# Optimization experiments

Measured on AMD Instinct MI355X. Metric: run time of the kernel, lower is better.

The kernel has to match this reference:

```python
import jax, jax.numpy as jnp
import numpy as np

B, C, H, W = 2, 512, 48, 48
HEADS = 8          # head_dim = C // HEADS = 64
GROUPS = 32        # min(32, ceil(512/4)) = 32
EPS = 1e-5


def setup_inputs() -> dict:
    key = jax.random.key(0)
    ks = jax.random.split(key, 5)
    return {
        "x": jax.random.normal(ks[0], (B, C, H, W), jnp.float32),
        "gn_w": jnp.ones((C,), jnp.float32),
        "gn_b": jnp.zeros((C,), jnp.float32),
        # 1x1 convs stored as [out, in] matrices
        "qkv_w": jax.random.normal(ks[1], (3 * C, C), jnp.float32) / np.float32(np.sqrt(C)),
        "qkv_b": jax.random.normal(ks[2], (3 * C,), jnp.float32) * 0.01,
        "proj_w": jax.random.normal(ks[3], (C, C), jnp.float32) / np.float32(np.sqrt(C)),
        "proj_b": jax.random.normal(ks[4], (C,), jnp.float32) * 0.01,
    }


def _group_norm(x, w, b):
    b_, c_, h_, w_ = x.shape
    xg = x.reshape(b_, GROUPS, c_ // GROUPS, h_, w_)
    mean = xg.mean(axis=(2, 3, 4), keepdims=True)
    var = xg.var(axis=(2, 3, 4), keepdims=True)  # biased, matches F.group_norm
    xn = ((xg - mean) * jax.lax.rsqrt(var + EPS)).reshape(b_, c_, h_, w_)
    return xn * w[None, :, None, None] + b[None, :, None, None]


def reference(x, gn_w, gn_b, qkv_w, qkv_b, proj_w, proj_b):
    bx, cx, hx, wx = x.shape
    d = cx // HEADS
    n = hx * wx
    xn = _group_norm(x, gn_w, gn_b)
    # qkv 1x1 conv -> [B, 3C, H, W]
    y = jnp.einsum('oc,bchw->bohw', qkv_w, xn) + qkv_b[None, :, None, None]
    # torch: y.reshape(B*heads, d, 3, N).unbind(2)  (channel layout: head, chan, qkv)
    qkv = y.reshape(bx * HEADS, d, 3, n)
    q, k, v = qkv[:, :, 0, :], qkv[:, :, 1, :], qkv[:, :, 2, :]
    scale = np.float32(1.0 / np.sqrt(d))
    # AttentionOp: fp32 QK^T + softmax over keys (axis=2)
    w_attn = jax.nn.softmax(jnp.einsum('ncq,nck->nqk', q, k * scale), axis=2)
    a = jnp.einsum('nqk,nck->ncq', w_attn, v).reshape(bx, cx, hx, wx)
    out = jnp.einsum('oc,bchw->bohw', proj_w, a) + proj_b[None, :, None, None]
    return out + x
```

## Files before the change

kernel.cpp:

```cpp
#include <hip/hip_runtime.h>

typedef __bf16 bf16;
typedef __bf16 bf16x8 __attribute__((ext_vector_type(8)));
typedef __bf16 bf16x4 __attribute__((ext_vector_type(4)));
typedef float f32x4 __attribute__((ext_vector_type(4)));

#define B_ 2
#define C_ 512
#define HW_ 2304
#define GROUPS_ 32
#define CPG_ 16
#define EPS_ 1e-5f
#define THR_ 8.0f
#define LOG2E_ 1.44269504f
#define EXP2(x) __builtin_amdgcn_exp2f(x)

__device__ __forceinline__ void gload_lds16(const bf16* g, bf16* l) {
  __builtin_amdgcn_global_load_lds((const __attribute__((address_space(1))) void*)g,
                                   (__attribute__((address_space(3))) void*)l, 16, 0, 0);
}

__global__ __launch_bounds__(256) void gn_stats_part_k(const float* __restrict__ x,
                                                       float* __restrict__ ps,
                                                       float* __restrict__ pss) {
  int blk = blockIdx.x;
  int bg = blk >> 3, seg = blk & 7;
  const int n4 = CPG_ * HW_ / 4 / 8;
  const float4* p = (const float4*)(x + (long)bg * CPG_ * HW_) + (long)seg * n4;
  float s = 0.f, ss = 0.f;
  for (int i = threadIdx.x; i < n4; i += 256) {
    float4 v = p[i];
    s += v.x + v.y + v.z + v.w;
    ss += v.x * v.x + v.y * v.y + v.z * v.z + v.w * v.w;
  }
#pragma unroll
  for (int d = 1; d < 64; d <<= 1) { s += __shfl_xor(s, d); ss += __shfl_xor(ss, d); }
  __shared__ float rs[4], rss[4];
  int wave = threadIdx.x >> 6, lane = threadIdx.x & 63;
  if (lane == 0) { rs[wave] = s; rss[wave] = ss; }
  __syncthreads();
  if (threadIdx.x == 0) {
    ps[blk] = rs[0] + rs[1] + rs[2] + rs[3];
    pss[blk] = rss[0] + rss[1] + rss[2] + rss[3];
  }
}

__global__ __launch_bounds__(256) void gn_apply_k(const float* __restrict__ x,
                                                  const float* __restrict__ gw,
                                                  const float* __restrict__ gb,
                                                  const float* __restrict__ ps,
                                                  const float* __restrict__ pss,
                                                  bf16* __restrict__ xnT) {
  int n0 = blockIdx.x * 64, c0 = blockIdx.y * 32, b = blockIdx.z;
  int nn = n0 + (threadIdx.x & 63);
  int cb = c0 + ((threadIdx.x >> 6) << 3);
  int gi = b * GROUPS_ + (cb >> 4);
  float s = 0.f, ss = 0.f;
#pragma unroll
  for (int k = 0; k < 8; ++k) { s += ps[gi * 8 + k]; ss += pss[gi * 8 + k]; }
  const float invN = 1.0f / (float)(CPG_ * HW_);
  float mu = s * invN;
  float var = ss * invN - mu * mu;
  float rstd = rsqrtf(var + EPS_);
  bf16x8 o;
#pragma unroll
  for (int j = 0; j < 8; ++j) {
    int c = cb + j;
    float sc = rstd * gw[c];
    float sh = gb[c] - mu * sc;
    float v = x[((long)b * C_ + c) * HW_ + nn];
    o[j] = (bf16)(v * sc + sh);
  }
  *(bf16x8*)&xnT[((long)b * HW_ + nn) * C_ + cb] = o;
}

__global__ __launch_bounds__(256) void prep_w_k(const float* __restrict__ qkv_w,
                                                const float* __restrict__ qkv_b,
                                                const float* __restrict__ proj_w,
                                                bf16* __restrict__ wqk,
                                                bf16* __restrict__ wv,
                                                bf16* __restrict__ wp,
                                                float* __restrict__ bqk,
                                                float* __restrict__ bv) {
  int idx = blockIdx.x * 256 + threadIdx.x;
  int r = idx >> 9, c = idx & 511;
  {
    int src = (r < 512) ? 3 * r : 3 * (r - 512) + 1;
    float sc = (r < 512) ? 0.125f * LOG2E_ : 1.0f;
    wqk[idx] = (bf16)(qkv_w[(long)src * 512 + c] * sc);
  }
  if (r < 512) {
    wv[idx] = (bf16)(qkv_w[(long)(3 * r + 2) * 512 + c]);
    wp[idx] = (bf16)(proj_w[idx]);
  }
  if (idx < 1024) {
    int src = (idx < 512) ? 3 * idx : 3 * (idx - 512) + 1;
    float sc = (idx < 512) ? 0.125f * LOG2E_ : 1.0f;
    bqk[idx] = qkv_b[src] * sc;
  }
  if (idx < 512) bv[idx] = qkv_b[3 * idx + 2];
}

template <int BIAS_MODE, bool RESID, typename OUT_T>
__global__ __launch_bounds__(256) void gemm_k(const bf16* __restrict__ A,
                                              const bf16* __restrict__ BT,
                                              const float* __restrict__ bias,
                                              const float* __restrict__ resid,
                                              OUT_T* __restrict__ Cc,
                                              int M, int N,
                                              long sA, long sBT, long sC) {
  constexpr int KK = 512;
  constexpr int NSTEP = KK >> 5;
  int b = blockIdx.z;
  A += sA * b;
  BT += sBT * b;
  Cc += sC * b;
  const float* R = RESID ? (resid + sC * b) : nullptr;
  int m0 = blockIdx.y * 64, n0 = blockIdx.x * 64;
  int tid = threadIdx.x, lane = tid & 63, wave = tid >> 6;
  int wm = (wave >> 1) << 5, wn = (wave & 1) << 5;
  int fr = lane & 15, kg = (lane >> 4) << 3;
  __shared__ __align__(16) bf16 As[3][64 * 32];
  __shared__ __align__(16) bf16 Bs[3][64 * 32];
  int sr = tid >> 2, sc = (tid & 3) << 3;
  const bf16* gA = A + (long)(m0 + sr) * KK + sc;
  const bf16* gB = BT + (long)(n0 + sr) * KK + sc;
  f32x4 acc[2][2] = {};
  gload_lds16(gA, &As[0][tid * 8]);
  gload_lds16(gB, &Bs[0][tid * 8]);
  gload_lds16(gA + 32, &As[1][tid * 8]);
  gload_lds16(gB + 32, &Bs[1][tid * 8]);
  asm volatile("s_waitcnt vmcnt(2)" ::: "memory");
  __builtin_amdgcn_s_barrier();
#pragma unroll
  for (int t = 0; t < NSTEP; ++t) {
    const int cur = t % 3;
    if (t + 2 < NSTEP) {
      const int nb = (t + 2) % 3;
      int k0 = (t + 2) << 5;
      gload_lds16(gA + k0, &As[nb][tid * 8]);
      gload_lds16(gB + k0, &Bs[nb][tid * 8]);
    }
    bf16x8 a0 = *(bf16x8*)&As[cur][(wm + fr) * 32 + kg];
    bf16x8 a1 = *(bf16x8*)&As[cur][(wm + 16 + fr) * 32 + kg];
    bf16x8 b0 = *(bf16x8*)&Bs[cur][(wn + fr) * 32 + kg];
    bf16x8 b1 = *(bf16x8*)&Bs[cur][(wn + 16 + fr) * 32 + kg];
    acc[0][0] = __builtin_amdgcn_mfma_f32_16x16x32_bf16(a0, b0, acc[0][0], 0, 0, 0);
    acc[0][1] = __builtin_amdgcn_mfma_f32_16x16x32_bf16(a0, b1, acc[0][1], 0, 0, 0);
    acc[1][0] = __builtin_amdgcn_mfma_f32_16x16x32_bf16(a1, b0, acc[1][0], 0, 0, 0);
    acc[1][1] = __builtin_amdgcn_mfma_f32_16x16x32_bf16(a1, b1, acc[1][1], 0, 0, 0);
    if (t + 2 < NSTEP) {
      asm volatile("s_waitcnt vmcnt(2) lgkmcnt(0)" ::: "memory");
    } else if (t + 1 < NSTEP) {
      asm volatile("s_waitcnt vmcnt(0) lgkmcnt(0)" ::: "memory");
    }
    if (t + 1 < NSTEP) __builtin_amdgcn_s_barrier();
  }
  int rbase = (lane >> 4) << 2;
#pragma unroll
  for (int mi = 0; mi < 2; ++mi)
#pragma unroll
    for (int nj = 0; nj < 2; ++nj)
#pragma unroll
      for (int reg = 0; reg < 4; ++reg) {
        int row = m0 + wm + (mi << 4) + rbase + reg;
        int col = n0 + wn + (nj << 4) + fr;
        float v = acc[mi][nj][reg];
        if (BIAS_MODE == 1) v += bias[row];
        if (BIAS_MODE == 2) v += bias[col];
        if (RESID) v += R[(long)row * N + col];
        Cc[(long)row * N + col] = (OUT_T)v;
      }
}

template <int NS>
__global__ __launch_bounds__(512) void attn_k(const bf16* __restrict__ yT,
                                              const bf16* __restrict__ V,
                                              bf16* __restrict__ Op,
                                              float* __restrict__ Mp,
                                              float* __restrict__ Lp) {
  const int n = HW_;
  constexpr int NT = (HW_ / NS) / 64;
  int bh = blockIdx.y, b = bh >> 3, h = bh & 7;
  int split = blockIdx.z;
  int q0 = blockIdx.x * 128;
  int kbeg = split * (n / NS);
  int tid = threadIdx.x, lane = tid & 63, wave = tid >> 6;
  int fr = lane & 15, g = lane >> 4, kg = g << 3;
  const bf16* yTb = yT + (long)b * n * 1024;
  const bf16* Vb = V + ((long)b * C_ + h * 64) * n;
  const bf16* Kb = yTb + 512 + h * 64;

  int qrow = q0 + (wave << 4) + fr;
  const bf16* qp = yTb + (long)qrow * 1024 + h * 64;
  bf16x8 qf0 = *(const bf16x8*)(qp + kg);
  bf16x8 qf1 = *(const bf16x8*)(qp + 32 + kg);

  __shared__ __align__(16) bf16 Kt[2][64][64];
  __shared__ __align__(16) bf16 Vt[2][64][64];

  int o0 = ((g + fr) & 7) << 3;
  int o1 = ((4 + g + fr) & 7) << 3;

  float m_run = -1e30f, l_run = 0.f;
  f32x4 oacc[4] = {};

  int r0 = tid >> 3;
  int ck = tid & 7;
  int c0e = ck << 3;
  int pk = ((ck + r0) & 7) << 3;
  int vs = (c0e & 32) | ((c0e & 8) << 1) | ((c0e & 16) >> 2);
  int cv = vs >> 3, sub = vs & 7;
  int pv0 = (((cv + r0) & 7) << 3) + sub;
  int pv1 = (((cv + 1 + r0) & 7) << 3) + sub;

  const bf16* kptr = Kb + (long)(kbeg + r0) * 1024 + c0e;
  const bf16* vptr = Vb + (long)r0 * n + kbeg + c0e;
  uint4 rk = *(const uint4*)kptr;
  uint4 rv = *(const uint4*)vptr;
  *(uint4*)&Kt[0][r0][pk] = rk;
  *(uint2*)&Vt[0][r0][pv0] = make_uint2(rv.x, rv.y);
  *(uint2*)&Vt[0][r0][pv1] = make_uint2(rv.z, rv.w);
  kptr += 64 * 1024;
  vptr += 64;
  rk = *(const uint4*)kptr;
  rv = *(const uint4*)vptr;
  __syncthreads();

  for (int t = 0; t < NT; ++t) {
    int cur = t & 1;
    f32x4 s[4] = {};
    __builtin_amdgcn_s_setprio(1);
#pragma unroll
    for (int nj = 0; nj < 4; ++nj) {
      bf16x8 kf0 = *(bf16x8*)&Kt[cur][(nj << 4) + fr][o0];
      bf16x8 kf1 = *(bf16x8*)&Kt[cur][(nj << 4) + fr][o1];
      s[nj] = __builtin_amdgcn_mfma_f32_16x16x32_bf16(kf0, qf0, s[nj], 0, 0, 0);
      s[nj] = __builtin_amdgcn_mfma_f32_16x16x32_bf16(kf1, qf1, s[nj], 0, 0, 0);
    }
    __builtin_amdgcn_s_setprio(0);
    if (t + 1 < NT) {
      int nb = cur ^ 1;
      *(uint4*)&Kt[nb][r0][pk] = rk;
      *(uint2*)&Vt[nb][r0][pv0] = make_uint2(rv.x, rv.y);
      *(uint2*)&Vt[nb][r0][pv1] = make_uint2(rv.z, rv.w);
      if (t + 2 < NT) {
        kptr += 64 * 1024;
        vptr += 64;
        rk = *(const uint4*)kptr;
        rv = *(const uint4*)vptr;
      }
    }
    float pm = fmaxf(fmaxf(s[0][0], s[0][1]), fmaxf(s[0][2], s[0][3]));
#pragma unroll
    for (int nj = 1; nj < 4; ++nj)
      pm = fmaxf(pm, fmaxf(fmaxf(s[nj][0], s[nj][1]), fmaxf(s[nj][2], s[nj][3])));
    pm = fmaxf(pm, __shfl_xor(pm, 16));
    pm = fmaxf(pm, __shfl_xor(pm, 32));
    if (__any(pm > m_run + THR_)) {
      float mn = fmaxf(m_run, pm);
      float corr = EXP2(m_run - mn);
      m_run = mn;
      l_run *= corr;
#pragma unroll
      for (int dj = 0; dj < 4; ++dj)
#pragma unroll
        for (int r = 0; r < 4; ++r) oacc[dj][r] *= corr;
    }
    float ls = 0.f;
    bf16x8 pa0, pa1;
#pragma unroll
    for (int r = 0; r < 4; ++r) {
      float p0 = EXP2(s[0][r] - m_run);
      float p1 = EXP2(s[1][r] - m_run);
      float p2 = EXP2(s[2][r] - m_run);
      float p3 = EXP2(s[3][r] - m_run);
      ls += (p0 + p1) + (p2 + p3);
      pa0[r] = (bf16)p0;
      pa0[4 + r] = (bf16)p1;
      pa1[r] = (bf16)p2;
      pa1[4 + r] = (bf16)p3;
    }
    ls += __shfl_xor(ls, 16);
    ls += __shfl_xor(ls, 32);
    l_run += ls;
    __builtin_amdgcn_s_setprio(1);
#pragma unroll
    for (int dj = 0; dj < 4; ++dj) {
      bf16x8 vf0 = *(bf16x8*)&Vt[cur][(dj << 4) + fr][o0];
      bf16x8 vf1 = *(bf16x8*)&Vt[cur][(dj << 4) + fr][o1];
      oacc[dj] = __builtin_amdgcn_mfma_f32_16x16x32_bf16(vf0, pa0, oacc[dj], 0, 0, 0);
      oacc[dj] = __builtin_amdgcn_mfma_f32_16x16x32_bf16(vf1, pa1, oacc[dj], 0, 0, 0);
    }
    __builtin_amdgcn_s_setprio(0);
    __syncthreads();
  }
  long orow = (long)(split * 16 + bh) * n + q0 + (wave << 4) + fr;
#pragma unroll
  for (int dj = 0; dj < 4; ++dj) {
    bf16x4 ov = {(bf16)oacc[dj][0], (bf16)oacc[dj][1], (bf16)oacc[dj][2], (bf16)oacc[dj][3]};
    *(bf16x4*)&Op[orow * 64 + (dj << 4) + (g << 2)] = ov;
  }
  if (g == 0) {
    Mp[orow] = m_run;
    Lp[orow] = l_run;
  }
}

template <int NS>
__global__ __launch_bounds__(256) void attn_merge_k(const bf16* __restrict__ Op,
                                                    const float* __restrict__ Mp,
                                                    const float* __restrict__ Lp,
                                                    bf16* __restrict__ aT) {
  int bh = blockIdx.y, b = bh >> 3, h = bh & 7;
  int gi = blockIdx.x * 256 + threadIdx.x;
  int nrow = gi >> 3, dd8 = (gi & 7) << 3;
  long idx[NS];
  float mm = -1e30f;
#pragma unroll
  for (int s = 0; s < NS; ++s) {
    idx[s] = (long)(s * 16 + bh) * HW_ + nrow;
    mm = fmaxf(mm, Mp[idx[s]]);
  }
  float l = 0.f, w[NS];
#pragma unroll
  for (int s = 0; s < NS; ++s) {
    w[s] = EXP2(Mp[idx[s]] - mm);
    l += Lp[idx[s]] * w[s];
  }
  float invl = 1.f / l;
  float oaccf[8] = {};
#pragma unroll
  for (int s = 0; s < NS; ++s) {
    bf16x8 o = *(const bf16x8*)&Op[idx[s] * 64 + dd8];
    float ws = w[s] * invl;
#pragma unroll
    for (int j = 0; j < 8; ++j) oaccf[j] += (float)o[j] * ws;
  }
  bf16x8 o;
#pragma unroll
  for (int j = 0; j < 8; ++j) o[j] = (bf16)oaccf[j];
  *(bf16x8*)&aT[((long)b * HW_ + nrow) * C_ + h * 64 + dd8] = o;
}

extern "C" void kernel_launch(void* const* d_in, const int* in_sizes, int n_in,
                              void* d_out, int out_size, void* d_ws, size_t ws_size,
                              hipStream_t stream) {
  const float* x = (const float*)d_in[0];
  const float* gn_w = (const float*)d_in[1];
  const float* gn_b = (const float*)d_in[2];
  const float* qkv_w = (const float*)d_in[3];
  const float* qkv_b = (const float*)d_in[4];
  const float* proj_w = (const float*)d_in[5];
  const float* proj_b = (const float*)d_in[6];
  float* out = (float*)d_out;

  char* ws = (char*)d_ws;
  float* ps = (float*)ws;   ws += 2048;
  float* pss = (float*)ws;  ws += 2048;
  float* bqk = (float*)ws;  ws += 4096;
  float* bv = (float*)ws;   ws += 2048;
  bf16* wqk = (bf16*)ws;    ws += 1024l * 512 * 2;
  bf16* wv = (bf16*)ws;     ws += 512l * 512 * 2;
  bf16* wp = (bf16*)ws;     ws += 512l * 512 * 2;
  bf16* xnT = (bf16*)ws;    ws += 2l * HW_ * 512 * 2;
  bf16* yT = (bf16*)ws;     ws += 2l * HW_ * 1024 * 2;
  bf16* v = (bf16*)ws;      ws += 2l * 512 * HW_ * 2;
  bf16* aT = (bf16*)ws;     ws += 2l * HW_ * 512 * 2;
  bf16* Op = (bf16*)ws;
  size_t base_used = (size_t)(ws - (char*)d_ws);
  size_t need4 = base_used + 4ull * 16 * HW_ * 64 * 2 + 2ull * 4 * 16 * HW_ * 4;
  int NS = (ws_size >= need4) ? 4 : 2;
  ws += (size_t)NS * 16 * HW_ * 64 * 2;
  float* Mp = (float*)ws;   ws += (size_t)NS * 16 * HW_ * 4;
  float* Lp = (float*)ws;   ws += (size_t)NS * 16 * HW_ * 4;

  gn_stats_part_k<<<512, 256, 0, stream>>>(x, ps, pss);
  prep_w_k<<<2048, 256, 0, stream>>>(qkv_w, qkv_b, proj_w, wqk, wv, wp, bqk, bv);
  gn_apply_k<<<dim3(36, 16, 2), 256, 0, stream>>>(x, gn_w, gn_b, ps, pss, xnT);
  gemm_k<2, false, bf16><<<dim3(16, 36, 2), 256, 0, stream>>>(
      xnT, wqk, bqk, nullptr, yT, 2304, 1024, (long)HW_ * 512, 0, (long)HW_ * 1024);
  gemm_k<1, false, bf16><<<dim3(36, 8, 2), 256, 0, stream>>>(
      wv, xnT, bv, nullptr, v, 512, 2304, 0, (long)HW_ * 512, 512l * HW_);
  if (NS == 4) {
    attn_k<4><<<dim3(18, 16, 4), 512, 0, stream>>>(yT, v, Op, Mp, Lp);
    attn_merge_k<4><<<dim3(72, 16), 256, 0, stream>>>(Op, Mp, Lp, aT);
  } else {
    attn_k<2><<<dim3(18, 16, 2), 512, 0, stream>>>(yT, v, Op, Mp, Lp);
    attn_merge_k<2><<<dim3(72, 16), 256, 0, stream>>>(Op, Mp, Lp, aT);
  }
  gemm_k<1, true, float><<<dim3(36, 8, 2), 256, 0, stream>>>(
      wp, aT, proj_b, x, out, 512, 2304, 0, (long)HW_ * 512, 512l * HW_);
}
```

Baseline: 93.93 us.

## Merge GN stats with weight prep and widen GEMM K-step with swizzled LDS

The GroupNorm partial-stats kernel and the weight-conversion kernel are merged into one launch, with the work chosen by block index, to save a launch. The GEMM K-step per pipeline stage doubles from 32 to 64, halving the number of barriers and iterations. LDS tiles use an XOR-like rotation swizzle to avoid bank conflicts on the wider rows. This adds more LDS per block (three stages of 64x64 for each operand), which may reduce occupancy.

```diff
diff --git a/kernel.cpp b/kernel.cpp
--- a/kernel.cpp
+++ b/kernel.cpp
@@ -20,28 +20,56 @@
                                    (__attribute__((address_space(3))) void*)l, 16, 0, 0);
 }
 
-__global__ __launch_bounds__(256) void gn_stats_part_k(const float* __restrict__ x,
-                                                       float* __restrict__ ps,
-                                                       float* __restrict__ pss) {
+__global__ __launch_bounds__(256) void pre_k(const float* __restrict__ x,
+                                             const float* __restrict__ qkv_w,
+                                             const float* __restrict__ qkv_b,
+                                             const float* __restrict__ proj_w,
+                                             float* __restrict__ ps,
+                                             float* __restrict__ pss,
+                                             bf16* __restrict__ wqk,
+                                             bf16* __restrict__ wv,
+                                             bf16* __restrict__ wp,
+                                             float* __restrict__ bqk,
+                                             float* __restrict__ bv) {
   int blk = blockIdx.x;
-  int bg = blk >> 3, seg = blk & 7;
-  const int n4 = CPG_ * HW_ / 4 / 8;
-  const float4* p = (const float4*)(x + (long)bg * CPG_ * HW_) + (long)seg * n4;
-  float s = 0.f, ss = 0.f;
-  for (int i = threadIdx.x; i < n4; i += 256) {
-    float4 v = p[i];
-    s += v.x + v.y + v.z + v.w;
-    ss += v.x * v.x + v.y * v.y + v.z * v.z + v.w * v.w;
-  }
-#pragma unroll
-  for (int d = 1; d < 64; d <<= 1) { s += __shfl_xor(s, d); ss += __shfl_xor(ss, d); }
-  __shared__ float rs[4], rss[4];
-  int wave = threadIdx.x >> 6, lane = threadIdx.x & 63;
-  if (lane == 0) { rs[wave] = s; rss[wave] = ss; }
-  __syncthreads();
-  if (threadIdx.x == 0) {
-    ps[blk] = rs[0] + rs[1] + rs[2] + rs[3];
-    pss[blk] = rss[0] + rss[1] + rss[2] + rss[3];
+  if (blk < 512) {
+    int bg = blk >> 3, seg = blk & 7;
+    const int n4 = CPG_ * HW_ / 4 / 8;
+    const float4* p = (const float4*)(x + (long)bg * CPG_ * HW_) + (long)seg * n4;
+    float s = 0.f, ss = 0.f;
+    for (int i = threadIdx.x; i < n4; i += 256) {
+      float4 v = p[i];
+      s += v.x + v.y + v.z + v.w;
+      ss += v.x * v.x + v.y * v.y + v.z * v.z + v.w * v.w;
+    }
+#pragma unroll
+    for (int d = 1; d < 64; d <<= 1) { s += __shfl_xor(s, d); ss += __shfl_xor(ss, d); }
+    __shared__ float rs[4], rss[4];
+    int wave = threadIdx.x >> 6, lane = threadIdx.x & 63;
+    if (lane == 0) { rs[wave] = s; rss[wave] = ss; }
+    __syncthreads();
+    if (threadIdx.x == 0) {
+      ps[blk] = rs[0] + rs[1] + rs[2] + rs[3];
+      pss[blk] = rss[0] + rss[1] + rss[2] + rss[3];
+    }
+  } else {
+    int idx = (blk - 512) * 256 + threadIdx.x;
+    int r = idx >> 9, c = idx & 511;
+    {
+      int src = (r < 512) ? 3 * r : 3 * (r - 512) + 1;
+      float sc = (r < 512) ? 0.125f * LOG2E_ : 1.0f;
+      wqk[idx] = (bf16)(qkv_w[(long)src * 512 + c] * sc);
+    }
+    if (r < 512) {
+      wv[idx] = (bf16)(qkv_w[(long)(3 * r + 2) * 512 + c]);
+      wp[idx] = (bf16)(proj_w[idx]);
+    }
+    if (idx < 1024) {
+      int src = (idx < 512) ? 3 * idx : 3 * (idx - 512) + 1;
+      float sc = (idx < 512) ? 0.125f * LOG2E_ : 1.0f;
+      bqk[idx] = qkv_b[src] * sc;
+    }
+    if (idx < 512) bv[idx] = qkv_b[3 * idx + 2];
   }
 }
 
@@ -74,33 +102,6 @@
   *(bf16x8*)&xnT[((long)b * HW_ + nn) * C_ + cb] = o;
 }
 
-__global__ __launch_bounds__(256) void prep_w_k(const float* __restrict__ qkv_w,
-                                                const float* __restrict__ qkv_b,
-                                                const float* __restrict__ proj_w,
-                                                bf16* __restrict__ wqk,
-                                                bf16* __restrict__ wv,
-                                                bf16* __restrict__ wp,
-                                                float* __restrict__ bqk,
-                                                float* __restrict__ bv) {
-  int idx = blockIdx.x * 256 + threadIdx.x;
-  int r = idx >> 9, c = idx & 511;
-  {
-    int src = (r < 512) ? 3 * r : 3 * (r - 512) + 1;
-    float sc = (r < 512) ? 0.125f * LOG2E_ : 1.0f;
-    wqk[idx] = (bf16)(qkv_w[(long)src * 512 + c] * sc);
-  }
-  if (r < 512) {
-    wv[idx] = (bf16)(qkv_w[(long)(3 * r + 2) * 512 + c]);
-    wp[idx] = (bf16)(proj_w[idx]);
-  }
-  if (idx < 1024) {
-    int src = (idx < 512) ? 3 * idx : 3 * (idx - 512) + 1;
-    float sc = (idx < 512) ? 0.125f * LOG2E_ : 1.0f;
-    bqk[idx] = qkv_b[src] * sc;
-  }
-  if (idx < 512) bv[idx] = qkv_b[3 * idx + 2];
-}
-
 template <int BIAS_MODE, bool RESID, typename OUT_T>
 __global__ __launch_bounds__(256) void gemm_k(const bf16* __restrict__ A,
                                               const bf16* __restrict__ BT,
@@ -110,7 +111,7 @@
                                               int M, int N,
                                               long sA, long sBT, long sC) {
   constexpr int KK = 512;
-  constexpr int NSTEP = KK >> 5;
+  constexpr int NSTEP = KK >> 6;
   int b = blockIdx.z;
   A += sA * b;
   BT += sBT * b;
@@ -119,38 +120,55 @@
   int m0 = blockIdx.y * 64, n0 = blockIdx.x * 64;
   int tid = threadIdx.x, lane = tid & 63, wave = tid >> 6;
   int wm = (wave >> 1) << 5, wn = (wave & 1) << 5;
-  int fr = lane & 15, kg = (lane >> 4) << 3;
-  __shared__ __align__(16) bf16 As[3][64 * 32];
-  __shared__ __align__(16) bf16 Bs[3][64 * 32];
-  int sr = tid >> 2, sc = (tid & 3) << 3;
-  const bf16* gA = A + (long)(m0 + sr) * KK + sc;
-  const bf16* gB = BT + (long)(n0 + sr) * KK + sc;
+  int fr = lane & 15, g = lane >> 4;
+  __shared__ __align__(16) bf16 As[3][64 * 64];
+  __shared__ __align__(16) bf16 Bs[3][64 * 64];
+  int sr = tid >> 3;
+  int swz = (((tid & 7) + sr) & 7) << 3;
+  const bf16* gA = A + (long)(m0 + sr) * KK + swz;
+  const bf16* gB = BT + (long)(n0 + sr) * KK + swz;
+  int o0 = ((g - fr) & 7) << 3;
+  int o1 = ((4 + g - fr) & 7) << 3;
   f32x4 acc[2][2] = {};
   gload_lds16(gA, &As[0][tid * 8]);
+  gload_lds16(gA + 32 * KK, &As[0][2048 + tid * 8]);
   gload_lds16(gB, &Bs[0][tid * 8]);
-  gload_lds16(gA + 32, &As[1][tid * 8]);
-  gload_lds16(gB + 32, &Bs[1][tid * 8]);
-  asm volatile("s_waitcnt vmcnt(2)" ::: "memory");
+  gload_lds16(gB + 32 * KK, &Bs[0][2048 + tid * 8]);
+  gload_lds16(gA + 64, &As[1][tid * 8]);
+  gload_lds16(gA + 32 * KK + 64, &As[1][2048 + tid * 8]);
+  gload_lds16(gB + 64, &Bs[1][tid * 8]);
+  gload_lds16(gB + 32 * KK + 64, &Bs[1][2048 + tid * 8]);
+  asm volatile("s_waitcnt vmcnt(4)" ::: "memory");
   __builtin_amdgcn_s_barrier();
 #pragma unroll
   for (int t = 0; t < NSTEP; ++t) {
     const int cur = t % 3;
     if (t + 2 < NSTEP) {
       const int nb = (t + 2) % 3;
-      int k0 = (t + 2) << 5;
+      int k0 = (t + 2) << 6;
       gload_lds16(gA + k0, &As[nb][tid * 8]);
+      gload_lds16(gA + 32 * KK + k0, &As[nb][2048 + tid * 8]);
       gload_lds16(gB + k0, &Bs[nb][tid * 8]);
-    }
-    bf16x8 a0 = *(bf16x8*)&As[cur][(wm + fr) * 32 + kg];
-    bf16x8 a1 = *(bf16x8*)&As[cur][(wm + 16 + fr) * 32 + kg];
-    bf16x8 b0 = *(bf16x8*)&Bs[cur][(wn + fr) * 32 + kg];
-    bf16x8 b1 = *(bf16x8*)&Bs[cur][(wn + 16 + fr) * 32 + kg];
-    acc[0][0] = __builtin_amdgcn_mfma_f32_16x16x32_bf16(a0, b0, acc[0][0], 0, 0, 0);
-    acc[0][1] = __builtin_amdgcn_mfma_f32_16x16x32_bf16(a0, b1, acc[0][1], 0, 0, 0);
-    acc[1][0] = __builtin_amdgcn_mfma_f32_16x16x32_bf16(a1, b0, acc[1][0], 0, 0, 0);
-    acc[1][1] = __builtin_amdgcn_mfma_f32_16x16x32_bf16(a1, b1, acc[1][1], 0, 0, 0);
+      gload_lds16(gB + 32 * KK + k0, &Bs[nb][2048 + tid * 8]);
+    }
+    bf16x8 a00 = *(bf16x8*)&As[cur][(wm + fr) * 64 + o0];
+    bf16x8 a01 = *(bf16x8*)&As[cur][(wm + fr) * 64 + o1];
+    bf16x8 a10 = *(bf16x8*)&As[cur][(wm + 16 + fr) * 64 + o0];
+    bf16x8 a11 = *(bf16x8*)&As[cur][(wm + 16 + fr) * 64 + o1];
+    bf16x8 b00 = *(bf16x8*)&Bs[cur][(wn + fr) * 64 + o0];
+    bf16x8 b01 = *(bf16x8*)&Bs[cur][(wn + fr) * 64 + o1];
+    bf16x8 b10 = *(bf16x8*)&Bs[cur][(wn + 16 + fr) * 64 + o0];
+    bf16x8 b11 = *(bf16x8*)&Bs[cur][(wn + 16 + fr) * 64 + o1];
+    acc[0][0] = __builtin_amdgcn_mfma_f32_16x16x32_bf16(a00, b00, acc[0][0], 0, 0, 0);
+    acc[0][0] = __builtin_amdgcn_mfma_f32_16x16x32_bf16(a01, b01, acc[0][0], 0, 0, 0);
+    acc[0][1] = __builtin_amdgcn_mfma_f32_16x16x32_bf16(a00, b10, acc[0][1], 0, 0, 0);
+    acc[0][1] = __builtin_amdgcn_mfma_f32_16x16x32_bf16(a01, b11, acc[0][1], 0, 0, 0);
+    acc[1][0] = __builtin_amdgcn_mfma_f32_16x16x32_bf16(a10, b00, acc[1][0], 0, 0, 0);
+    acc[1][0] = __builtin_amdgcn_mfma_f32_16x16x32_bf16(a11, b01, acc[1][0], 0, 0, 0);
+    acc[1][1] = __builtin_amdgcn_mfma_f32_16x16x32_bf16(a10, b10, acc[1][1], 0, 0, 0);
+    acc[1][1] = __builtin_amdgcn_mfma_f32_16x16x32_bf16(a11, b11, acc[1][1], 0, 0, 0);
     if (t + 2 < NSTEP) {
-      asm volatile("s_waitcnt vmcnt(2) lgkmcnt(0)" ::: "memory");
+      asm volatile("s_waitcnt vmcnt(4) lgkmcnt(0)" ::: "memory");
     } else if (t + 1 < NSTEP) {
       asm volatile("s_waitcnt vmcnt(0) lgkmcnt(0)" ::: "memory");
     }
@@ -375,8 +393,7 @@
   float* Mp = (float*)ws;   ws += (size_t)NS * 16 * HW_ * 4;
   float* Lp = (float*)ws;   ws += (size_t)NS * 16 * HW_ * 4;
 
-  gn_stats_part_k<<<512, 256, 0, stream>>>(x, ps, pss);
-  prep_w_k<<<2048, 256, 0, stream>>>(qkv_w, qkv_b, proj_w, wqk, wv, wp, bqk, bv);
+  pre_k<<<2560, 256, 0, stream>>>(x, qkv_w, qkv_b, proj_w, ps, pss, wqk, wv, wp, bqk, bv);
   gn_apply_k<<<dim3(36, 16, 2), 256, 0, stream>>>(x, gn_w, gn_b, ps, pss, xnT);
   gemm_k<2, false, bf16><<<dim3(16, 36, 2), 256, 0, stream>>>(
       xnT, wqk, bqk, nullptr, yT, 2304, 1024, (long)HW_ * 512, 0, (long)HW_ * 1024);
```

After: 85.68 us. 8.8% less time.
